# Performance work log

Hardware: AMD Instinct MI355X
Metric: run time of the kernel (lower is better)

The kernel has to match this reference:

```python
import jax, jax.numpy as jnp
import numpy as np

B, N, DIM = 1, 4096, 1024
HEADS, DIM_HEAD = 12, 8
POST_LOG_SCALE = 1.0
SCALE = DIM_HEAD ** -0.5


def setup_inputs() -> dict:
    key = jax.random.key(0)
    kx, kw = jax.random.split(key)
    x = jax.random.normal(kx, (B, N, DIM), dtype=jnp.float32)
    # torch nn.Linear(dim, heads*dim_head*2, bias=False) weight: [2*heads*dim_head, dim]
    W = jax.random.normal(kw, (2 * HEADS * DIM_HEAD, DIM), dtype=jnp.float32) * (DIM ** -0.5)
    return {"x": x, "W": W}


def reference(x, W):
    b, n, _ = x.shape
    # linear: x @ W^T -> [b, n, 2*h*d]; rearrange '(qk h d) -> qk b h n d'
    proj = jnp.einsum('bnc,oc->bno', x, W)
    proj = proj.reshape(b, n, 2, HEADS, DIM_HEAD)
    q = jnp.transpose(proj[:, :, 0], (0, 2, 1, 3))  # [b, h, n, d]
    k = jnp.transpose(proj[:, :, 1], (0, 2, 1, 3))  # [b, h, n, d]
    # small-d QK matmul -> [b, h, n, n]
    gates = jnp.einsum('bhid,bhjd->bhij', q, k) * SCALE
    gates = jax.nn.log_sigmoid(gates) * POST_LOG_SCALE
    # causal_mask = triu(ones, diagonal=0); masked_fill -> zero on/above diagonal
    i = jnp.arange(n)[:, None]
    j = jnp.arange(n)[None, :]
    keep = j < i  # strictly lower-triangular entries survive
    gates = jnp.where(keep, gates, 0.0)
    # flip-cumsum-flip == reverse cumulative sum along last axis
    gates = jax.lax.cumsum(gates, axis=3, reverse=True)
    return gates
```

## Files before the change

kernel.cpp:

```cpp
#include <hip/hip_runtime.h>

#define NTOK 4096
#define DIMC 1024
#define HEADS 12
#define DH 8
#define QSCALE 0.35355339059327373f
#define LOG2E  1.4426950408889634f
#define LN2    0.6931471805599453f

typedef float f4 __attribute__((ext_vector_type(4)));

#define KOFF (HEADS * NTOK * DH)

__global__ __launch_bounds__(256) void k1_proj(const float* __restrict__ x,
                                               const float* __restrict__ W,
                                               float* __restrict__ qk) {
    __shared__ float xs[8 * 1028];
    const int t = threadIdx.x;
    const int row0 = blockIdx.x * 8;

    const f4* x4 = (const f4*)(x + (size_t)row0 * DIMC);
    #pragma unroll
    for (int i = 0; i < 8; ++i) {
        int f = t + i * 256;
        int r = f >> 8;
        int c4 = f & 255;
        f4 v = x4[f];
        *(f4*)(&xs[r * 1028 + c4 * 4]) = v;
    }
    __syncthreads();

    const int g  = t >> 2;
    const int rg = t & 3;

    float acc[2][3];
    #pragma unroll
    for (int a = 0; a < 2; ++a)
        #pragma unroll
        for (int m = 0; m < 3; ++m) acc[a][m] = 0.f;

    const float* w0 = W + (size_t)(3 * g) * DIMC;
    #pragma unroll 2
    for (int c = 0; c < DIMC; c += 4) {
        f4 w[3];
        #pragma unroll
        for (int m = 0; m < 3; ++m)
            w[m] = *(const f4*)(w0 + (size_t)m * DIMC + c);
        #pragma unroll
        for (int a = 0; a < 2; ++a) {
            f4 xv = *(const f4*)(&xs[(rg * 2 + a) * 1028 + c]);
            #pragma unroll
            for (int m = 0; m < 3; ++m) {
                acc[a][m] = fmaf(xv.x, w[m].x,
                            fmaf(xv.y, w[m].y,
                            fmaf(xv.z, w[m].z,
                            fmaf(xv.w, w[m].w, acc[a][m]))));
            }
        }
    }

    #pragma unroll
    for (int m = 0; m < 3; ++m) {
        int o   = 3 * g + m;
        int qkf = (o >= 96) ? 1 : 0;
        int oo  = o - 96 * qkf;
        int h   = oo >> 3;
        int d   = oo & 7;
        #pragma unroll
        for (int a = 0; a < 2; ++a) {
            int n = row0 + rg * 2 + a;
            float v = acc[a][m];
            if (!qkf) {
                qk[((size_t)h * NTOK + n) * DH + d] = v * QSCALE;
            } else {
                qk[KOFF + ((size_t)h * DH + d) * NTOK + n] = v;
            }
        }
    }
}

__device__ __forceinline__ float log_sigmoid(float s) {
    float mn = fminf(s, 0.f);
    float z  = __builtin_amdgcn_exp2f(fabsf(s) * -LOG2E);
    return mn - LN2 * __builtin_amdgcn_logf(1.f + z);
}

__global__ __launch_bounds__(256) void k2_gates(const float* __restrict__ qk,
                                                float* __restrict__ out) {
    const int bid  = blockIdx.x;
    const int h    = bid >> 9;
    const int i0   = (bid & 511) << 3;
    const int t    = threadIdx.x;
    const int lane = t & 63;
    const int wid  = t >> 6;
    const int r0   = i0 + 2 * wid;

    const float* qrow = qk + ((size_t)h * NTOK + r0) * DH;
    float qa[8], qb[8];
    #pragma unroll
    for (int d = 0; d < 8; ++d) { qa[d] = qrow[d]; qb[d] = qrow[DH + d]; }

    const float* ks = qk + KOFF + (size_t)h * DH * NTOK;
    float* o0 = out + ((size_t)h * NTOK + r0) * NTOK;
    float* o1 = o0 + NTOK;

    const int ccmax = r0 >> 8;

    f4 z = (f4)(0.f);
    for (int cc = 15; cc > ccmax; --cc) {
        const int j0 = cc * 256 + 4 * lane;
        __builtin_nontemporal_store(z, (f4*)(o0 + j0));
        __builtin_nontemporal_store(z, (f4*)(o1 + j0));
    }

    float carry0 = 0.f, carry1 = 0.f;
    for (int cc = ccmax; cc >= 0; --cc) {
        const int j0 = cc * 256 + 4 * lane;

        f4 kv[8];
        #pragma unroll
        for (int d = 0; d < 8; ++d)
            kv[d] = *(const f4*)(ks + (size_t)d * NTOK + j0);

        float a0 = 0.f, a1 = 0.f, a2 = 0.f, a3 = 0.f;
        float b0 = 0.f, b1 = 0.f, b2 = 0.f, b3 = 0.f;
        #pragma unroll
        for (int d = 0; d < 8; ++d) {
            a0 = fmaf(qa[d], kv[d].x, a0);
            a1 = fmaf(qa[d], kv[d].y, a1);
            a2 = fmaf(qa[d], kv[d].z, a2);
            a3 = fmaf(qa[d], kv[d].w, a3);
            b0 = fmaf(qb[d], kv[d].x, b0);
            b1 = fmaf(qb[d], kv[d].y, b1);
            b2 = fmaf(qb[d], kv[d].z, b2);
            b3 = fmaf(qb[d], kv[d].w, b3);
        }

        float g0[4], g1[4];
        g0[0] = (j0 + 0 < r0) ? log_sigmoid(a0) : 0.f;
        g0[1] = (j0 + 1 < r0) ? log_sigmoid(a1) : 0.f;
        g0[2] = (j0 + 2 < r0) ? log_sigmoid(a2) : 0.f;
        g0[3] = (j0 + 3 < r0) ? log_sigmoid(a3) : 0.f;
        const int r1 = r0 + 1;
        g1[0] = (j0 + 0 < r1) ? log_sigmoid(b0) : 0.f;
        g1[1] = (j0 + 1 < r1) ? log_sigmoid(b1) : 0.f;
        g1[2] = (j0 + 2 < r1) ? log_sigmoid(b2) : 0.f;
        g1[3] = (j0 + 3 < r1) ? log_sigmoid(b3) : 0.f;

        g0[2] += g0[3]; g0[1] += g0[2]; g0[0] += g0[1];
        g1[2] += g1[3]; g1[1] += g1[2]; g1[0] += g1[1];
        const float t0 = g0[0], t1 = g1[0];

        float s0 = t0, s1 = t1;
        #pragma unroll
        for (int off = 1; off < 64; off <<= 1) {
            float v0 = __shfl_down(s0, off, 64);
            float v1 = __shfl_down(s1, off, 64);
            if (lane + off < 64) { s0 += v0; s1 += v1; }
        }
        const float base0 = (s0 - t0) + carry0;
        const float base1 = (s1 - t1) + carry1;
        carry0 += __shfl(s0, 0, 64);
        carry1 += __shfl(s1, 0, 64);

        f4 v0, v1;
        v0.x = g0[0] + base0; v0.y = g0[1] + base0;
        v0.z = g0[2] + base0; v0.w = g0[3] + base0;
        v1.x = g1[0] + base1; v1.y = g1[1] + base1;
        v1.z = g1[2] + base1; v1.w = g1[3] + base1;
        __builtin_nontemporal_store(v0, (f4*)(o0 + j0));
        __builtin_nontemporal_store(v1, (f4*)(o1 + j0));
    }
}

extern "C" void kernel_launch(void* const* d_in, const int* in_sizes, int n_in,
                              void* d_out, int out_size, void* d_ws, size_t ws_size,
                              hipStream_t stream) {
    const float* x = (const float*)d_in[0];
    const float* W = (const float*)d_in[1];
    float* out = (float*)d_out;
    float* qk  = (float*)d_ws;

    hipLaunchKernelGGL(k1_proj, dim3(NTOK / 8), dim3(256), 0, stream, x, W, qk);
    hipLaunchKernelGGL(k2_gates, dim3(HEADS * NTOK / 8), dim3(256), 0, stream, qk, out);
}
```

Baseline: 209.3 us.

## Fold log2 scaling into Q, use packed FMAs, peel diagonal chunk, tile K

Q is pre-scaled by log2(e) so log-sigmoid works in base 2 and the LN2 factor is applied once after the scan. The QK dot products and the projection use 2-wide packed FMAs (v_pk_fma_f32). The diagonal chunk is peeled so that full chunks skip the mask compares, and the carry is broadcast with readfirstlane. K is stored in 256-token blocks so each chunk's loads are contiguous. Rounding changes slightly from the reordered arithmetic. The kernel is dominated by output stores, so the compute savings may be partly hidden.

After: 203.4 us. 2.8% less time.

```diff
diff --git a/kernel.cpp b/kernel.cpp
--- a/kernel.cpp
+++ b/kernel.cpp
@@ -7,8 +7,10 @@
 #define QSCALE 0.35355339059327373f
 #define LOG2E  1.4426950408889634f
 #define LN2    0.6931471805599453f
+#define QPRE   (QSCALE * LOG2E)
 
 typedef float f4 __attribute__((ext_vector_type(4)));
+typedef float f2 __attribute__((ext_vector_type(2)));
 
 #define KOFF (HEADS * NTOK * DH)
 
@@ -33,11 +35,11 @@
     const int g  = t >> 2;
     const int rg = t & 3;
 
-    float acc[2][3];
+    f2 acc[2][3];
     #pragma unroll
     for (int a = 0; a < 2; ++a)
         #pragma unroll
-        for (int m = 0; m < 3; ++m) acc[a][m] = 0.f;
+        for (int m = 0; m < 3; ++m) acc[a][m] = (f2)(0.f);
 
     const float* w0 = W + (size_t)(3 * g) * DIMC;
     #pragma unroll 2
@@ -51,10 +53,8 @@
             f4 xv = *(const f4*)(&xs[(rg * 2 + a) * 1028 + c]);
             #pragma unroll
             for (int m = 0; m < 3; ++m) {
-                acc[a][m] = fmaf(xv.x, w[m].x,
-                            fmaf(xv.y, w[m].y,
-                            fmaf(xv.z, w[m].z,
-                            fmaf(xv.w, w[m].w, acc[a][m]))));
+                acc[a][m] = __builtin_elementwise_fma(xv.xy, w[m].xy, acc[a][m]);
+                acc[a][m] = __builtin_elementwise_fma(xv.zw, w[m].zw, acc[a][m]);
             }
         }
     }
@@ -69,20 +69,20 @@
         #pragma unroll
         for (int a = 0; a < 2; ++a) {
             int n = row0 + rg * 2 + a;
-            float v = acc[a][m];
+            float v = acc[a][m].x + acc[a][m].y;
             if (!qkf) {
-                qk[((size_t)h * NTOK + n) * DH + d] = v * QSCALE;
+                qk[((size_t)h * NTOK + n) * DH + d] = v * QPRE;
             } else {
-                qk[KOFF + ((size_t)h * DH + d) * NTOK + n] = v;
+                qk[KOFF + (((size_t)h * 16 + (n >> 8)) * DH + d) * 256 + (n & 255)] = v;
             }
         }
     }
 }
 
-__device__ __forceinline__ float log_sigmoid(float s) {
-    float mn = fminf(s, 0.f);
-    float z  = __builtin_amdgcn_exp2f(fabsf(s) * -LOG2E);
-    return mn - LN2 * __builtin_amdgcn_logf(1.f + z);
+__device__ __forceinline__ float lsig2(float u) {
+    float mn = fminf(u, 0.f);
+    float z  = __builtin_amdgcn_exp2f(-fabsf(u));
+    return mn - __builtin_amdgcn_logf(1.f + z);
 }
 
 __global__ __launch_bounds__(256) void k2_gates(const float* __restrict__ qk,
@@ -94,63 +94,61 @@
     const int lane = t & 63;
     const int wid  = t >> 6;
     const int r0   = i0 + 2 * wid;
+    const int r1   = r0 + 1;
 
     const float* qrow = qk + ((size_t)h * NTOK + r0) * DH;
-    float qa[8], qb[8];
-    #pragma unroll
-    for (int d = 0; d < 8; ++d) { qa[d] = qrow[d]; qb[d] = qrow[DH + d]; }
-
-    const float* ks = qk + KOFF + (size_t)h * DH * NTOK;
+    f2 q0s[8], q1s[8];
+    #pragma unroll
+    for (int d = 0; d < 8; ++d) {
+        q0s[d] = (f2)(qrow[d]);
+        q1s[d] = (f2)(qrow[DH + d]);
+    }
+
+    const float* kh = qk + KOFF + (size_t)h * (16 * DH * 256) + 4 * lane;
     float* o0 = out + ((size_t)h * NTOK + r0) * NTOK;
     float* o1 = o0 + NTOK;
 
-    const int ccmax = r0 >> 8;
+    const int cb = r0 >> 8;
 
     f4 z = (f4)(0.f);
-    for (int cc = 15; cc > ccmax; --cc) {
+    for (int cc = 15; cc > cb; --cc) {
         const int j0 = cc * 256 + 4 * lane;
         __builtin_nontemporal_store(z, (f4*)(o0 + j0));
         __builtin_nontemporal_store(z, (f4*)(o1 + j0));
     }
 
-    float carry0 = 0.f, carry1 = 0.f;
-    for (int cc = ccmax; cc >= 0; --cc) {
-        const int j0 = cc * 256 + 4 * lane;
+    float carry0, carry1;
+
+    {
+        const int j0 = cb * 256 + 4 * lane;
+        const float* kc = kh + (size_t)cb * (DH * 256);
 
         f4 kv[8];
         #pragma unroll
-        for (int d = 0; d < 8; ++d)
-            kv[d] = *(const f4*)(ks + (size_t)d * NTOK + j0);
-
-        float a0 = 0.f, a1 = 0.f, a2 = 0.f, a3 = 0.f;
-        float b0 = 0.f, b1 = 0.f, b2 = 0.f, b3 = 0.f;
+        for (int d = 0; d < 8; ++d) kv[d] = *(const f4*)(kc + d * 256);
+
+        f2 A0 = (f2)(0.f), B0 = (f2)(0.f), A1 = (f2)(0.f), B1 = (f2)(0.f);
         #pragma unroll
         for (int d = 0; d < 8; ++d) {
-            a0 = fmaf(qa[d], kv[d].x, a0);
-            a1 = fmaf(qa[d], kv[d].y, a1);
-            a2 = fmaf(qa[d], kv[d].z, a2);
-            a3 = fmaf(qa[d], kv[d].w, a3);
-            b0 = fmaf(qb[d], kv[d].x, b0);
-            b1 = fmaf(qb[d], kv[d].y, b1);
-            b2 = fmaf(qb[d], kv[d].z, b2);
-            b3 = fmaf(qb[d], kv[d].w, b3);
+            A0 = __builtin_elementwise_fma(kv[d].xy, q0s[d], A0);
+            B0 = __builtin_elementwise_fma(kv[d].zw, q0s[d], B0);
+            A1 = __builtin_elementwise_fma(kv[d].xy, q1s[d], A1);
+            B1 = __builtin_elementwise_fma(kv[d].zw, q1s[d], B1);
         }
 
         float g0[4], g1[4];
-        g0[0] = (j0 + 0 < r0) ? log_sigmoid(a0) : 0.f;
-        g0[1] = (j0 + 1 < r0) ? log_sigmoid(a1) : 0.f;
-        g0[2] = (j0 + 2 < r0) ? log_sigmoid(a2) : 0.f;
-        g0[3] = (j0 + 3 < r0) ? log_sigmoid(a3) : 0.f;
-        const int r1 = r0 + 1;
-        g1[0] = (j0 + 0 < r1) ? log_sigmoid(b0) : 0.f;
-        g1[1] = (j0 + 1 < r1) ? log_sigmoid(b1) : 0.f;
-        g1[2] = (j0 + 2 < r1) ? log_sigmoid(b2) : 0.f;
-        g1[3] = (j0 + 3 < r1) ? log_sigmoid(b3) : 0.f;
+        g0[0] = (j0 + 0 < r0) ? lsig2(A0.x) : 0.f;
+        g0[1] = (j0 + 1 < r0) ? lsig2(A0.y) : 0.f;
+        g0[2] = (j0 + 2 < r0) ? lsig2(B0.x) : 0.f;
+        g0[3] = (j0 + 3 < r0) ? lsig2(B0.y) : 0.f;
+        g1[0] = (j0 + 0 < r1) ? lsig2(A1.x) : 0.f;
+        g1[1] = (j0 + 1 < r1) ? lsig2(A1.y) : 0.f;
+        g1[2] = (j0 + 2 < r1) ? lsig2(B1.x) : 0.f;
+        g1[3] = (j0 + 3 < r1) ? lsig2(B1.y) : 0.f;
 
         g0[2] += g0[3]; g0[1] += g0[2]; g0[0] += g0[1];
         g1[2] += g1[3]; g1[1] += g1[2]; g1[0] += g1[1];
         const float t0 = g0[0], t1 = g1[0];
-
         float s0 = t0, s1 = t1;
         #pragma unroll
         for (int off = 1; off < 64; off <<= 1) {
@@ -158,18 +156,63 @@
             float v1 = __shfl_down(s1, off, 64);
             if (lane + off < 64) { s0 += v0; s1 += v1; }
         }
+        const float base0 = s0 - t0;
+        const float base1 = s1 - t1;
+        carry0 = __builtin_amdgcn_readfirstlane(s0);
+        carry1 = __builtin_amdgcn_readfirstlane(s1);
+
+        f4 gv0 = {g0[0], g0[1], g0[2], g0[3]};
+        f4 gv1 = {g1[0], g1[1], g1[2], g1[3]};
+        f4 ov0 = (gv0 + base0) * LN2;
+        f4 ov1 = (gv1 + base1) * LN2;
+        __builtin_nontemporal_store(ov0, (f4*)(o0 + j0));
+        __builtin_nontemporal_store(ov1, (f4*)(o1 + j0));
+    }
+
+    for (int cc = cb - 1; cc >= 0; --cc) {
+        const int j0 = cc * 256 + 4 * lane;
+        const float* kc = kh + (size_t)cc * (DH * 256);
+
+        f4 kv[8];
+        #pragma unroll
+        for (int d = 0; d < 8; ++d) kv[d] = *(const f4*)(kc + d * 256);
+
+        f2 A0 = (f2)(0.f), B0 = (f2)(0.f), A1 = (f2)(0.f), B1 = (f2)(0.f);
+        #pragma unroll
+        for (int d = 0; d < 8; ++d) {
+            A0 = __builtin_elementwise_fma(kv[d].xy, q0s[d], A0);
+            B0 = __builtin_elementwise_fma(kv[d].zw, q0s[d], B0);
+            A1 = __builtin_elementwise_fma(kv[d].xy, q1s[d], A1);
+            B1 = __builtin_elementwise_fma(kv[d].zw, q1s[d], B1);
+        }
+
+        float g0[4], g1[4];
+        g0[0] = lsig2(A0.x); g0[1] = lsig2(A0.y);
+        g0[2] = lsig2(B0.x); g0[3] = lsig2(B0.y);
+        g1[0] = lsig2(A1.x); g1[1] = lsig2(A1.y);
+        g1[2] = lsig2(B1.x); g1[3] = lsig2(B1.y);
+
+        g0[2] += g0[3]; g0[1] += g0[2]; g0[0] += g0[1];
+        g1[2] += g1[3]; g1[1] += g1[2]; g1[0] += g1[1];
+        const float t0 = g0[0], t1 = g1[0];
+        float s0 = t0, s1 = t1;
+        #pragma unroll
+        for (int off = 1; off < 64; off <<= 1) {
+            float v0 = __shfl_down(s0, off, 64);
+            float v1 = __shfl_down(s1, off, 64);
+            if (lane + off < 64) { s0 += v0; s1 += v1; }
+        }
         const float base0 = (s0 - t0) + carry0;
         const float base1 = (s1 - t1) + carry1;
-        carry0 += __shfl(s0, 0, 64);
-        carry1 += __shfl(s1, 0, 64);
-
-        f4 v0, v1;
-        v0.x = g0[0] + base0; v0.y = g0[1] + base0;
-        v0.z = g0[2] + base0; v0.w = g0[3] + base0;
-        v1.x = g1[0] + base1; v1.y = g1[1] + base1;
-        v1.z = g1[2] + base1; v1.w = g1[3] + base1;
-        __builtin_nontemporal_store(v0, (f4*)(o0 + j0));
-        __builtin_nontemporal_store(v1, (f4*)(o1 + j0));
+        carry0 += __builtin_amdgcn_readfirstlane(s0);
+        carry1 += __builtin_amdgcn_readfirstlane(s1);
+
+        f4 gv0 = {g0[0], g0[1], g0[2], g0[3]};
+        f4 gv1 = {g1[0], g1[1], g1[2], g1[3]};
+        f4 ov0 = (gv0 + base0) * LN2;
+        f4 ov1 = (gv1 + base1) * LN2;
+        __builtin_nontemporal_store(ov0, (f4*)(o0 + j0));
+        __builtin_nontemporal_store(ov1, (f4*)(o1 + j0));
     }
 }
 
```
